# Kernel optimization log

Hardware: AMD Instinct MI355X
Metric: run time of the kernel (lower is better)

## Reference

```python
import jax, jax.numpy as jnp
import numpy as np

WS = 8       # window_size
SHIFT = 4    # shift_size
HEADS = 4

def _rel_pos_index():
    coords = np.stack(np.meshgrid(np.arange(WS), np.arange(WS), indexing='ij'))
    cf = coords.reshape(2, -1)                       # (2, N)
    rel = cf[:, :, None] - cf[:, None, :]            # (2, N, N)
    rel = rel.transpose(1, 2, 0).copy()              # (N, N, 2)
    rel[:, :, 0] += WS - 1
    rel[:, :, 1] += WS - 1
    rel[:, :, 0] *= 2 * WS - 1
    return jnp.asarray(rel.sum(-1))                  # (N, N) int

REL_IDX = _rel_pos_index()

def _conv(x, w, groups=1, pad=0):
    return jax.lax.conv_general_dilated(
        x, w, (1, 1), [(pad, pad), (pad, pad)],
        feature_group_count=groups,
        dimension_numbers=('NCHW', 'OIHW', 'NCHW'))

def _dwt_haar(x):
    # single-level orthonormal Haar on non-overlapping 2x2 blocks
    B, C, H, W = x.shape
    x = x.reshape(B, C, H // 2, 2, W // 2, 2)
    a = x[:, :, :, 0, :, 0]; b = x[:, :, :, 0, :, 1]
    c = x[:, :, :, 1, :, 0]; d = x[:, :, :, 1, :, 1]
    ll = (a + b + c + d) * 0.5
    lh = (a - b + c - d) * 0.5
    hl = (a + b - c - d) * 0.5
    hh = (a - b - c + d) * 0.5
    return ll, lh, hl, hh

def _idwt_haar(ll, lh, hl, hh):
    a = (ll + lh + hl + hh) * 0.5
    b = (ll - lh + hl - hh) * 0.5
    c = (ll + lh - hl - hh) * 0.5
    d = (ll - lh - hl + hh) * 0.5
    B, C, H2, W2 = ll.shape
    x = jnp.stack([jnp.stack([a, b], -1), jnp.stack([c, d], -1)], -2)  # (B,C,H2,W2,2row,2col)
    return x.transpose(0, 1, 2, 4, 3, 5).reshape(B, C, 2 * H2, 2 * W2)

def _window_partition(x):
    B, C, H, W = x.shape
    x = x.reshape(B, C, H // WS, WS, W // WS, WS).transpose(0, 2, 4, 1, 3, 5)
    return x.reshape(-1, C, WS, WS)

def _window_reverse(w, B, H, W):
    C = w.shape[1]
    x = w.reshape(B, H // WS, W // WS, C, WS, WS).transpose(0, 3, 1, 4, 2, 5)
    return x.reshape(B, C, H, W)

def setup_inputs() -> dict:
    key = jax.random.key(0)
    ks = jax.random.split(key, 8)
    dim = 64
    s = 0.05
    return {
        'x': jax.random.normal(ks[0], (8, dim, 256, 256), jnp.float32),
        'temperature': jnp.ones((HEADS, 1, 1), jnp.float32),
        'rel_bias_table': jax.random.normal(ks[1], ((2 * WS - 1) ** 2, HEADS), jnp.float32) * 0.02,
        'w_high1': jax.random.normal(ks[2], (2 * dim, dim, 3, 3), jnp.float32) * s,
        'w_high2': jax.random.normal(ks[3], (dim, 2 * dim, 1, 1), jnp.float32) * s,
        'w_highout': jax.random.normal(ks[4], (3 * dim, dim, 3, 3), jnp.float32) * s,
        'w_qkv': jax.random.normal(ks[5], (3 * dim, dim, 1, 1), jnp.float32) * s,
        'w_dwconv': jax.random.normal(ks[6], (3 * dim, 1, 3, 3), jnp.float32) * s,
        'w_proj': jax.random.normal(ks[7], (dim, dim, 1, 1), jnp.float32) * s,
    }

def reference(x, temperature, rel_bias_table, w_high1, w_high2, w_highout, w_qkv, w_dwconv, w_proj):
    B, C, H, W = x.shape
    ll, lh, hl, hh = _dwt_haar(x)
    # high-frequency modulation of v
    filt = jax.nn.relu(_conv(jnp.concatenate([lh, hl], 1), w_high1, groups=2, pad=1))
    filt = jax.nn.relu(_conv(filt, w_high2))
    qkv = _conv(_conv(ll, w_qkv), w_dwconv, groups=3 * C, pad=1)
    v_inp = qkv[:, 2 * C:]  # note: q,k from qkv are dead in the source; q=k come from shifted LL
    v = v_inp * filt + v_inp
    xs = jnp.roll(ll, (-SHIFT, -SHIFT), (2, 3))
    qw = _window_partition(xs)
    vw = _window_partition(v)
    Bw = qw.shape[0]; hd = C // HEADS; N = WS * WS
    q = qw.reshape(Bw, HEADS, hd, N)
    vv = vw.reshape(Bw, HEADS, hd, N)
    qn = q / jnp.maximum(jnp.linalg.norm(q, axis=-2, keepdims=True), 1e-12)
    # k == q in the source, so kn == qn
    attn = jnp.einsum('bhdn,bhdm->bhnm', qn, qn)                      # (Bw,h,N,N)
    bias = rel_bias_table[REL_IDX.reshape(-1)].reshape(N, N, HEADS).transpose(2, 0, 1)
    attn = (attn + bias[None]) * temperature[None]
    attn = jax.nn.softmax(attn, axis=-1)
    out = jnp.einsum('bhdm,bhnm->bhdn', vv, attn)                     # v @ attn^T
    out = out.reshape(Bw, C, WS, WS)
    out = _window_reverse(out, B, H // 2, W // 2)
    out = jnp.roll(out, (SHIFT, SHIFT), (2, 3))
    out = _conv(out, w_proj)
    yh = jax.nn.relu(_conv(jnp.concatenate([lh, hl, hh], 1), w_highout, groups=3, pad=1))
    lh2, hl2, hh2 = yh[:, :C], yh[:, C:2 * C], yh[:, 2 * C:]
    return _idwt_haar(out, lh2, hl2, hh2)
```

## Files before the change

kernel.cpp:

```cpp
#include <hip/hip_runtime.h>
#include <cstddef>

constexpr int HP  = 128 * 128;
constexpr long long S = 8LL * 64 * HP;

using short8 = __attribute__((ext_vector_type(8))) short;
using f32x4  = __attribute__((ext_vector_type(4))) float;

__device__ __forceinline__ unsigned short f2bf(float x) {
    union { float f; unsigned int u; } v{x};
    unsigned int r = v.u + 0x7FFFu + ((v.u >> 16) & 1u);
    return (unsigned short)(r >> 16);
}

__global__ __launch_bounds__(256) void k_dwt_fused(
        const float* __restrict__ x, float* __restrict__ ll,
        unsigned short* __restrict__ Tlh, unsigned short* __restrict__ Thl,
        unsigned short* __restrict__ Thh) {
    __shared__ unsigned short tlh[64][66];
    __shared__ unsigned short thl[64][66];
    __shared__ unsigned short thh[64][66];
    int b = blockIdx.y;
    int p0 = blockIdx.x * 64;
    int i = p0 >> 7, j0 = p0 & 127;
    int tid = threadIdx.x;
    {
        int p = tid & 63, c4 = tid >> 6;
        int j = j0 + p;
        const float* xb = x + (size_t)b * 64 * 65536;
#pragma unroll
        for (int k = 0; k < 16; ++k) {
            int c = c4 * 16 + k;
            const float* xp = xb + (size_t)c * 65536;
            float2 top = *(const float2*)(xp + (2 * i) * 256 + 2 * j);
            float2 bot = *(const float2*)(xp + (2 * i + 1) * 256 + 2 * j);
            float a = top.x, bb = top.y, cc = bot.x, dd = bot.y;
            ll[((size_t)b * 64 + c) * HP + p0 + p] = (a + bb + cc + dd) * 0.5f;
            tlh[c][p] = f2bf((a - bb + cc - dd) * 0.5f);
            thl[c][p] = f2bf((a + bb - cc - dd) * 0.5f);
            thh[c][p] = f2bf((a - bb - cc + dd) * 0.5f);
        }
    }
    __syncthreads();
    {
        int c = tid & 63, pq = tid >> 6;
        size_t ob = ((size_t)b * HP + p0) * 64;
#pragma unroll
        for (int k = 0; k < 16; ++k) {
            int p = pq * 16 + k;
            Tlh[ob + (size_t)p * 64 + c] = tlh[c][p];
            Thl[ob + (size_t)p * 64 + c] = thl[c][p];
            Thh[ob + (size_t)p * 64 + c] = thh[c][p];
        }
    }
}

__global__ __launch_bounds__(256) void k_wreorder(const float* __restrict__ w,
                                                  unsigned short* __restrict__ wr, int total) {
    int idx = blockIdx.x * 256 + threadIdx.x;
    if (idx >= total) return;
    int oc = idx / 576, rem = idx - oc * 576;
    int s = rem >> 6, ic = rem & 63;
    wr[idx] = f2bf(w[(oc * 64 + ic) * 9 + s]);
}

__global__ __launch_bounds__(256) void k_bias(const float* __restrict__ table,
                                              const float* __restrict__ temp,
                                              float* __restrict__ bd) {
    int idx = blockIdx.x * 256 + threadIdx.x;
    int h = idx >> 12, m = (idx >> 6) & 63, n = idx & 63;
    int i1 = n >> 3, j1 = n & 7, i2 = m >> 3, j2 = m & 7;
    int rel = (i1 - i2 + 7) * 15 + (j1 - j2 + 7);
    bd[idx] = table[rel * 4 + h] * temp[h];
}

#define ISTR 72
__global__ __launch_bounds__(256, 2) void k_conv3x3_mfma(
        const unsigned short* __restrict__ in,
        const unsigned short* __restrict__ wr,
        float* __restrict__ out, int out_ctot) {
    __shared__ __align__(16) unsigned short lin[324 * ISTR];
    __shared__ __align__(16) unsigned short lw[64 * ISTR];

    int tid = threadIdx.x;
    int b = blockIdx.y;
    int ty0 = (blockIdx.x >> 3) * 16, tx0 = (blockIdx.x & 7) * 16;

    const unsigned short* inb = in + (size_t)b * HP * 64;
    for (int idx = tid; idx < 324 * 8; idx += 256) {
        int pr = idx >> 3, l8 = idx & 7;
        int py = pr / 18, px = pr - py * 18;
        int gy = ty0 + py - 1, gx = tx0 + px - 1;
        uint4 v = make_uint4(0, 0, 0, 0);
        if (gy >= 0 && gy < 128 && gx >= 0 && gx < 128)
            v = *(const uint4*)(inb + ((size_t)(gy * 128 + gx)) * 64 + l8 * 8);
        *(uint4*)&lin[pr * ISTR + l8 * 8] = v;
    }

    int wv = tid >> 6;
    int lane = tid & 63;
    int n16 = lane & 15, quad = lane >> 4;

    f32x4 acc[4][4];
#pragma unroll
    for (int mt = 0; mt < 4; ++mt)
#pragma unroll
        for (int nt = 0; nt < 4; ++nt) acc[mt][nt] = (f32x4){0.f, 0.f, 0.f, 0.f};

    for (int s = 0; s < 9; ++s) {
        __syncthreads();
        for (int idx = tid; idx < 512; idx += 256) {
            int oc = idx >> 3, l8 = idx & 7;
            *(uint4*)&lw[oc * ISTR + l8 * 8] =
                *(const uint4*)(wr + oc * 576 + s * 64 + l8 * 8);
        }
        __syncthreads();
        int sy = s / 3, sx = s - sy * 3;
#pragma unroll
        for (int half = 0; half < 2; ++half) {
            int ic0 = half * 32 + quad * 8;
            short8 a[4], bf[4];
#pragma unroll
            for (int mt = 0; mt < 4; ++mt)
                a[mt] = *(const short8*)&lw[(mt * 16 + n16) * ISTR + ic0];
#pragma unroll
            for (int nt = 0; nt < 4; ++nt) {
                int py = 4 * wv + nt + sy;
                int px = n16 + sx;
                bf[nt] = *(const short8*)&lin[(py * 18 + px) * ISTR + ic0];
            }
#pragma unroll
            for (int mt = 0; mt < 4; ++mt)
#pragma unroll
                for (int nt = 0; nt < 4; ++nt)
                    acc[mt][nt] = __builtin_amdgcn_mfma_f32_16x16x32_bf16(
                        a[mt], bf[nt], acc[mt][nt], 0, 0, 0);
        }
    }

    int gx = tx0 + n16;
#pragma unroll
    for (int nt = 0; nt < 4; ++nt) {
        int gy = ty0 + 4 * wv + nt;
#pragma unroll
        for (int mt = 0; mt < 4; ++mt) {
#pragma unroll
            for (int r = 0; r < 4; ++r) {
                int oc = mt * 16 + quad * 4 + r;
                out[((size_t)b * out_ctot + oc) * HP + (size_t)gy * 128 + gx] =
                    fmaxf(acc[mt][nt][r], 0.0f);
            }
        }
    }
}

template <int IC, bool RELU>
__global__ __launch_bounds__(256) void k_conv1x1(const float* __restrict__ in,
                                                 const float* __restrict__ w,
                                                 float* __restrict__ out) {
    __shared__ float wl[IC * 16];
    int tid = threadIdx.x;
    int occ = blockIdx.y, b = blockIdx.z;
    for (int idx = tid; idx < IC * 16; idx += 256) {
        int o = idx & 15, ic = idx >> 4;
        wl[idx] = w[(occ * 16 + o) * IC + ic];
    }
    __syncthreads();
    int p = blockIdx.x * 256 + tid;
    const float* inp = in + (size_t)b * IC * HP + p;
    float acc[16] = {};
    for (int ic = 0; ic < IC; ++ic) {
        float xv = inp[(size_t)ic * HP];
#pragma unroll
        for (int o = 0; o < 16; ++o) acc[o] += xv * wl[ic * 16 + o];
    }
    float* op = out + ((size_t)b * 64 + occ * 16) * HP + p;
#pragma unroll
    for (int o = 0; o < 16; ++o) op[o * HP] = RELU ? fmaxf(acc[o], 0.0f) : acc[o];
}

__global__ __launch_bounds__(256) void k_dwconv_v(const float* __restrict__ t,
                                                  const float* __restrict__ wdw,
                                                  const float* __restrict__ filt,
                                                  float* __restrict__ v) {
    long long idx = (long long)blockIdx.x * 256 + threadIdx.x;
    if (idx >= S) return;
    int j = (int)(idx & 127);
    int i = (int)((idx >> 7) & 127);
    int c = (int)((idx >> 14) & 63);
    long long bc = idx >> 14;
    const float* tp = t + bc * HP;
    const float* wp = wdw + c * 9;
    float acc = 0.0f;
#pragma unroll
    for (int ky = 0; ky < 3; ++ky) {
        int y = i + ky - 1;
        if (y < 0 || y >= 128) continue;
#pragma unroll
        for (int kx = 0; kx < 3; ++kx) {
            int x = j + kx - 1;
            if (x < 0 || x >= 128) continue;
            acc += tp[y * 128 + x] * wp[ky * 3 + kx];
        }
    }
    float f = filt[idx];
    v[idx] = acc * (1.0f + f);
}

union F16 { float4 v4[4]; float f[16]; };

__global__ __launch_bounds__(256, 4) void k_attn(const float* __restrict__ ll,
                                                 const float* __restrict__ v,
                                                 const float* __restrict__ bd,
                                                 const float* __restrict__ temp,
                                                 float* __restrict__ outbuf) {
    __shared__ __align__(16) float qs[64][64];
    __shared__ __align__(16) float vs[64][64];
    __shared__ __align__(16) float inv[4][64];
    int blk = blockIdx.x;
    int wj = blk & 15, wi = (blk >> 4) & 15, b = blk >> 8;
    int tid = threadIdx.x;

    for (int idx = tid; idx < 4096; idx += 256) {
        int c = idx >> 6, n = idx & 63;
        int i = n >> 3, j = n & 7;
        int qy = (wi * 8 + i + 4) & 127, qx = (wj * 8 + j + 4) & 127;
        int vy = wi * 8 + i, vx = wj * 8 + j;
        size_t cb = ((size_t)b * 64 + c) * HP;
        qs[c][n] = ll[cb + qy * 128 + qx];
        vs[c][n] = v[cb + vy * 128 + vx];
    }
    __syncthreads();

    int h = tid >> 6, n = tid & 63;
    float tscale = temp[h];
    float q[16];
    float ss = 0.0f;
#pragma unroll
    for (int d = 0; d < 16; ++d) {
        q[d] = qs[h * 16 + d][n];
        ss += q[d] * q[d];
    }
    float invn = 1.0f / fmaxf(sqrtf(ss), 1e-12f);
    inv[h][n] = invn;
    float qsc = invn * tscale;
#pragma unroll
    for (int d = 0; d < 16; ++d) q[d] *= qsc;
    __syncthreads();

    const float* bh = bd + (h << 12) + n;
    float mx = -1e30f, sum = 0.0f;
    float acc[16] = {};

    for (int c0 = 0; c0 < 64; c0 += 16) {
        float bb[16];
#pragma unroll
        for (int mm = 0; mm < 16; ++mm) bb[mm] = bh[(c0 + mm) * 64];

        float p[16] = {};
#pragma unroll
        for (int d = 0; d < 16; ++d) {
            F16 A;
            const float4* qr = (const float4*)&qs[h * 16 + d][c0];
            A.v4[0] = qr[0]; A.v4[1] = qr[1]; A.v4[2] = qr[2]; A.v4[3] = qr[3];
            float qd = q[d];
#pragma unroll
            for (int mm = 0; mm < 16; ++mm) p[mm] += qd * A.f[mm];
        }
        F16 I;
        const float4* ir = (const float4*)&inv[h][c0];
        I.v4[0] = ir[0]; I.v4[1] = ir[1]; I.v4[2] = ir[2]; I.v4[3] = ir[3];
        float cm = -1e30f;
#pragma unroll
        for (int mm = 0; mm < 16; ++mm) {
            p[mm] = p[mm] * I.f[mm] + bb[mm];
            cm = fmaxf(cm, p[mm]);
        }

        float nm = fmaxf(mx, cm);
        float scale = __expf(mx - nm);
        sum *= scale;
#pragma unroll
        for (int mm = 0; mm < 16; ++mm) {
            p[mm] = __expf(p[mm] - nm);
            sum += p[mm];
        }
#pragma unroll
        for (int d = 0; d < 16; ++d) acc[d] *= scale;

#pragma unroll
        for (int d = 0; d < 16; ++d) {
            F16 V;
            const float4* vr = (const float4*)&vs[h * 16 + d][c0];
            V.v4[0] = vr[0]; V.v4[1] = vr[1]; V.v4[2] = vr[2]; V.v4[3] = vr[3];
            float s = acc[d];
#pragma unroll
            for (int mm = 0; mm < 16; ++mm) s += p[mm] * V.f[mm];
            acc[d] = s;
        }
        mx = nm;
    }

    float rs = 1.0f / sum;
    int i1 = n >> 3, j1 = n & 7;
    int oy = (wi * 8 + i1 + 4) & 127, ox = (wj * 8 + j1 + 4) & 127;
#pragma unroll
    for (int d = 0; d < 16; ++d)
        outbuf[((size_t)b * 64 + h * 16 + d) * HP + oy * 128 + ox] = acc[d] * rs;
}

__global__ __launch_bounds__(256) void k_idwt(const float* __restrict__ ll, const float* __restrict__ lh,
                                              const float* __restrict__ hl, const float* __restrict__ hh,
                                              float* __restrict__ out) {
    long long idx = (long long)blockIdx.x * 256 + threadIdx.x;
    if (idx >= S) return;
    int j = (int)(idx & 127);
    int i = (int)((idx >> 7) & 127);
    long long bc = idx >> 14;
    float L = ll[idx], A = lh[idx], B = hl[idx], D = hh[idx];
    float a = (L + A + B + D) * 0.5f;
    float b = (L - A + B - D) * 0.5f;
    float c = (L + A - B - D) * 0.5f;
    float d = (L - A - B + D) * 0.5f;
    float* op = out + bc * 256 * 256;
    *(float2*)(op + (2 * i) * 256 + 2 * j) = make_float2(a, b);
    *(float2*)(op + (2 * i + 1) * 256 + 2 * j) = make_float2(c, d);
}

extern "C" void kernel_launch(void* const* d_in, const int* in_sizes, int n_in,
                              void* d_out, int out_size, void* d_ws, size_t ws_size,
                              hipStream_t stream) {
    const float* x        = (const float*)d_in[0];
    const float* temp     = (const float*)d_in[1];
    const float* table    = (const float*)d_in[2];
    const float* w_high1  = (const float*)d_in[3];
    const float* w_high2  = (const float*)d_in[4];
    const float* w_highout= (const float*)d_in[5];
    const float* w_qkv    = (const float*)d_in[6];
    const float* w_dwconv = (const float*)d_in[7];
    const float* w_proj   = (const float*)d_in[8];
    float* out = (float*)d_out;

    float* ws = (float*)d_ws;
    float* s0 = ws + 0 * S;
    float* s1 = ws + 1 * S;
    float* s2 = ws + 2 * S;
    float* s3 = ws + 3 * S;
    float* s4 = ws + 4 * S;
    float* s5 = ws + 5 * S;
    float* s6 = ws + 6 * S;
    float* s7 = ws + 7 * S;
    float* s8 = ws + 8 * S;

    unsigned short* T_lh = (unsigned short*)s4;
    unsigned short* T_hl = (unsigned short*)s4 + S;
    unsigned short* T_hh = (unsigned short*)s5;
    unsigned short* w_r1 = (unsigned short*)s5 + S;
    unsigned short* w_r2 = w_r1 + 128 * 576;
    float* bd = (float*)(w_r2 + 192 * 576);

    const int nblk = (int)(S / 256);
    dim3 b256(256);

    dim3 dg(HP / 64, 8);
    k_dwt_fused<<<dg, b256, 0, stream>>>(x, s0, T_lh, T_hl, T_hh);

    k_wreorder<<<(128 * 576 + 255) / 256, b256, 0, stream>>>(w_high1, w_r1, 128 * 576);
    k_wreorder<<<(192 * 576 + 255) / 256, b256, 0, stream>>>(w_highout, w_r2, 192 * 576);
    k_bias<<<64, b256, 0, stream>>>(table, temp, bd);

    dim3 cg(64, 8);
    k_conv3x3_mfma<<<cg, b256, 0, stream>>>(T_lh, w_r1,            s1,            128);
    k_conv3x3_mfma<<<cg, b256, 0, stream>>>(T_hl, w_r1 + 64 * 576, s1 + 64 * HP,  128);

    dim3 g1(64, 4, 8);
    k_conv1x1<128, true><<<g1, b256, 0, stream>>>(s1, w_high2, s6);

    k_conv1x1<64, false><<<g1, b256, 0, stream>>>(s0, w_qkv + 128 * 64, s7);

    k_dwconv_v<<<nblk, b256, 0, stream>>>(s7, w_dwconv + 128 * 9, s6, s6);

    k_attn<<<2048, b256, 0, stream>>>(s0, s6, bd, temp, s7);

    k_conv1x1<64, false><<<g1, b256, 0, stream>>>(s7, w_proj, s8);

    k_conv3x3_mfma<<<cg, b256, 0, stream>>>(T_lh, w_r2,             s1, 64);
    k_conv3x3_mfma<<<cg, b256, 0, stream>>>(T_hl, w_r2 + 64 * 576,  s2, 64);
    k_conv3x3_mfma<<<cg, b256, 0, stream>>>(T_hh, w_r2 + 128 * 576, s3, 64);

    k_idwt<<<nblk, b256, 0, stream>>>(s8, s1, s2, s3, out);
}
```

Before: 618.4 us.

## Fuse projection 1x1 conv into windowed attention, process window pairs, vectorize IDWT

The attention kernel now handles two adjacent windows per 512-thread block and loads Q/V with float4 reads, including a wrap-around path for the shifted region. It applies the w_proj 1x1 conv in shared memory before writing, which removes the separate conv1x1 launch and its intermediate read/write. The IDWT kernel handles two pixels per thread with float2 loads and float4 stores. Risks are higher shared-memory use (about 68KB) and register pressure at 512 threads, which may reduce occupancy.

```diff
diff --git a/kernel.cpp b/kernel.cpp
--- a/kernel.cpp
+++ b/kernel.cpp
@@ -209,40 +209,55 @@
 
 union F16 { float4 v4[4]; float f[16]; };
 
-__global__ __launch_bounds__(256, 4) void k_attn(const float* __restrict__ ll,
-                                                 const float* __restrict__ v,
-                                                 const float* __restrict__ bd,
-                                                 const float* __restrict__ temp,
-                                                 float* __restrict__ outbuf) {
-    __shared__ __align__(16) float qs[64][64];
-    __shared__ __align__(16) float vs[64][64];
-    __shared__ __align__(16) float inv[4][64];
+__global__ __launch_bounds__(512, 4) void k_attn2(const float* __restrict__ ll,
+                                                  const float* __restrict__ v,
+                                                  const float* __restrict__ bd,
+                                                  const float* __restrict__ temp,
+                                                  const float* __restrict__ wproj,
+                                                  float* __restrict__ outbuf) {
+    __shared__ __align__(16) float qs[64][132];
+    __shared__ __align__(16) float vs[64][132];
+    __shared__ __align__(16) float inv[4][128];
     int blk = blockIdx.x;
-    int wj = blk & 15, wi = (blk >> 4) & 15, b = blk >> 8;
+    int wjp = blk & 7, wi = (blk >> 3) & 15, b = blk >> 7;
     int tid = threadIdx.x;
 
-    for (int idx = tid; idx < 4096; idx += 256) {
-        int c = idx >> 6, n = idx & 63;
-        int i = n >> 3, j = n & 7;
-        int qy = (wi * 8 + i + 4) & 127, qx = (wj * 8 + j + 4) & 127;
-        int vy = wi * 8 + i, vx = wj * 8 + j;
+    for (int idx = tid; idx < 2048; idx += 512) {
+        int pq = idx & 31, c = idx >> 5;
+        int i = pq >> 2, xq = (pq & 3) * 4;
+        int w = xq >> 3;
+        int col = w * 64 + i * 8 + (xq & 7);
         size_t cb = ((size_t)b * 64 + c) * HP;
-        qs[c][n] = ll[cb + qy * 128 + qx];
-        vs[c][n] = v[cb + vy * 128 + vx];
-    }
-    __syncthreads();
-
-    int h = tid >> 6, n = tid & 63;
+        int qy = (wi * 8 + i + 4) & 127;
+        int qx0 = wjp * 16 + xq + 4;
+        int vy = wi * 8 + i, vx0 = wjp * 16 + xq;
+        float4 qv;
+        if (qx0 <= 124) {
+            qv = *(const float4*)(ll + cb + qy * 128 + qx0);
+        } else {
+            const float* lr = ll + cb + qy * 128;
+            qv = make_float4(lr[qx0 & 127], lr[(qx0 + 1) & 127],
+                             lr[(qx0 + 2) & 127], lr[(qx0 + 3) & 127]);
+        }
+        *(float4*)&qs[c][col] = qv;
+        *(float4*)&vs[c][col] = *(const float4*)(v + cb + vy * 128 + vx0);
+    }
+    __syncthreads();
+
+    int n = tid & 63;
+    int hw = tid >> 6;
+    int h = hw & 3, w = hw >> 2;
+    int wc = w << 6;
     float tscale = temp[h];
     float q[16];
     float ss = 0.0f;
 #pragma unroll
     for (int d = 0; d < 16; ++d) {
-        q[d] = qs[h * 16 + d][n];
+        q[d] = qs[h * 16 + d][wc + n];
         ss += q[d] * q[d];
     }
     float invn = 1.0f / fmaxf(sqrtf(ss), 1e-12f);
-    inv[h][n] = invn;
+    inv[h][wc + n] = invn;
     float qsc = invn * tscale;
 #pragma unroll
     for (int d = 0; d < 16; ++d) q[d] *= qsc;
@@ -261,14 +276,14 @@
 #pragma unroll
         for (int d = 0; d < 16; ++d) {
             F16 A;
-            const float4* qr = (const float4*)&qs[h * 16 + d][c0];
+            const float4* qr = (const float4*)&qs[h * 16 + d][wc + c0];
             A.v4[0] = qr[0]; A.v4[1] = qr[1]; A.v4[2] = qr[2]; A.v4[3] = qr[3];
             float qd = q[d];
 #pragma unroll
             for (int mm = 0; mm < 16; ++mm) p[mm] += qd * A.f[mm];
         }
         F16 I;
-        const float4* ir = (const float4*)&inv[h][c0];
+        const float4* ir = (const float4*)&inv[h][wc + c0];
         I.v4[0] = ir[0]; I.v4[1] = ir[1]; I.v4[2] = ir[2]; I.v4[3] = ir[3];
         float cm = -1e30f;
 #pragma unroll
@@ -291,7 +306,7 @@
 #pragma unroll
         for (int d = 0; d < 16; ++d) {
             F16 V;
-            const float4* vr = (const float4*)&vs[h * 16 + d][c0];
+            const float4* vr = (const float4*)&vs[h * 16 + d][wc + c0];
             V.v4[0] = vr[0]; V.v4[1] = vr[1]; V.v4[2] = vr[2]; V.v4[3] = vr[3];
             float s = acc[d];
 #pragma unroll
@@ -302,29 +317,59 @@
     }
 
     float rs = 1.0f / sum;
-    int i1 = n >> 3, j1 = n & 7;
-    int oy = (wi * 8 + i1 + 4) & 127, ox = (wj * 8 + j1 + 4) & 127;
-#pragma unroll
-    for (int d = 0; d < 16; ++d)
-        outbuf[((size_t)b * 64 + h * 16 + d) * HP + oy * 128 + ox] = acc[d] * rs;
+    __syncthreads();
+#pragma unroll
+    for (int d = 0; d < 16; ++d) qs[h * 16 + d][wc + n] = acc[d] * rs;
+    float* wl = &vs[0][0];
+    for (int idx = tid; idx < 4096; idx += 512) wl[idx] = wproj[idx];
+    __syncthreads();
+
+    int h2 = tid >> 7;
+    int p2 = tid & 127;
+    int i2 = p2 >> 4, xp = p2 & 15;
+    int col = ((xp >> 3) << 6) + (i2 << 3) + (xp & 7);
+    float po[16] = {};
+    for (int ic0 = 0; ic0 < 64; ic0 += 4) {
+        float x0 = qs[ic0 + 0][col];
+        float x1 = qs[ic0 + 1][col];
+        float x2 = qs[ic0 + 2][col];
+        float x3 = qs[ic0 + 3][col];
+#pragma unroll
+        for (int o = 0; o < 16; ++o) {
+            float4 wv = *(const float4*)&wl[(h2 * 16 + o) * 64 + ic0];
+            po[o] += x0 * wv.x + x1 * wv.y + x2 * wv.z + x3 * wv.w;
+        }
+    }
+    int oy = (wi * 8 + i2 + 4) & 127, ox = (wjp * 16 + xp + 4) & 127;
+#pragma unroll
+    for (int o = 0; o < 16; ++o)
+        outbuf[((size_t)b * 64 + h2 * 16 + o) * HP + oy * 128 + ox] = po[o];
 }
 
 __global__ __launch_bounds__(256) void k_idwt(const float* __restrict__ ll, const float* __restrict__ lh,
                                               const float* __restrict__ hl, const float* __restrict__ hh,
                                               float* __restrict__ out) {
-    long long idx = (long long)blockIdx.x * 256 + threadIdx.x;
-    if (idx >= S) return;
-    int j = (int)(idx & 127);
-    int i = (int)((idx >> 7) & 127);
-    long long bc = idx >> 14;
-    float L = ll[idx], A = lh[idx], B = hl[idx], D = hh[idx];
-    float a = (L + A + B + D) * 0.5f;
-    float b = (L - A + B - D) * 0.5f;
-    float c = (L + A - B - D) * 0.5f;
-    float d = (L - A - B + D) * 0.5f;
+    long long idx2 = (long long)blockIdx.x * 256 + threadIdx.x;
+    if (idx2 >= S / 2) return;
+    int j2 = (int)(idx2 & 63);
+    int i  = (int)((idx2 >> 6) & 127);
+    long long bc = idx2 >> 13;
+    long long base = bc * HP + i * 128 + 2 * j2;
+    float2 L = *(const float2*)(ll + base);
+    float2 A = *(const float2*)(lh + base);
+    float2 Bv = *(const float2*)(hl + base);
+    float2 D = *(const float2*)(hh + base);
+    float a0 = (L.x + A.x + Bv.x + D.x) * 0.5f;
+    float b0 = (L.x - A.x + Bv.x - D.x) * 0.5f;
+    float c0 = (L.x + A.x - Bv.x - D.x) * 0.5f;
+    float d0 = (L.x - A.x - Bv.x + D.x) * 0.5f;
+    float a1 = (L.y + A.y + Bv.y + D.y) * 0.5f;
+    float b1 = (L.y - A.y + Bv.y - D.y) * 0.5f;
+    float c1 = (L.y + A.y - Bv.y - D.y) * 0.5f;
+    float d1 = (L.y - A.y - Bv.y + D.y) * 0.5f;
     float* op = out + bc * 256 * 256;
-    *(float2*)(op + (2 * i) * 256 + 2 * j) = make_float2(a, b);
-    *(float2*)(op + (2 * i + 1) * 256 + 2 * j) = make_float2(c, d);
+    *(float4*)(op + (2 * i) * 256 + 4 * j2)     = make_float4(a0, b0, a1, b1);
+    *(float4*)(op + (2 * i + 1) * 256 + 4 * j2) = make_float4(c0, d0, c1, d1);
 }
 
 extern "C" void kernel_launch(void* const* d_in, const int* in_sizes, int n_in,
@@ -380,13 +425,11 @@
 
     k_dwconv_v<<<nblk, b256, 0, stream>>>(s7, w_dwconv + 128 * 9, s6, s6);
 
-    k_attn<<<2048, b256, 0, stream>>>(s0, s6, bd, temp, s7);
-
-    k_conv1x1<64, false><<<g1, b256, 0, stream>>>(s7, w_proj, s8);
+    k_attn2<<<1024, dim3(512), 0, stream>>>(s0, s6, bd, temp, w_proj, s8);
 
     k_conv3x3_mfma<<<cg, b256, 0, stream>>>(T_lh, w_r2,             s1, 64);
     k_conv3x3_mfma<<<cg, b256, 0, stream>>>(T_hl, w_r2 + 64 * 576,  s2, 64);
     k_conv3x3_mfma<<<cg, b256, 0, stream>>>(T_hh, w_r2 + 128 * 576, s3, 64);
 
-    k_idwt<<<nblk, b256, 0, stream>>>(s8, s1, s2, s3, out);
-}
+    k_idwt<<<(int)(S / 2 / 256), b256, 0, stream>>>(s8, s1, s2, s3, out);
+}
```

Measured after the change: 608.3 us. About the same (-1.6%).
